# Optimization experiments

Measured on AMD Instinct MI355X. Metric: run time of the kernel, lower is better.

Reference implementation:

```python
import jax, jax.numpy as jnp
import numpy as np

HIDDEN = 2048
VOCAB = 32768
SEQ = 4608
N_CHUNKS = 9
CAP = 30.0
IGNORE = -100


def setup_inputs() -> dict:
    key = jax.random.key(0)
    k1, k2, k3 = jax.random.split(key, 3)
    weight = (jax.random.normal(k1, (VOCAB, HIDDEN), dtype=jnp.float32) * 0.02).astype(jnp.bfloat16)
    hidden = jax.random.normal(k2, (1, SEQ, HIDDEN), dtype=jnp.float32)
    input_ids = jax.random.randint(k3, (1, SEQ), 0, VOCAB)
    attention_mask = jnp.ones((1, SEQ), dtype=jnp.int32)
    return {"weight": weight, "hidden": hidden, "input_ids": input_ids,
            "attention_mask": attention_mask}


def _build_labels(input_ids, attention_mask):
    # labels[t] = input_ids[t+1], masked-out positions and the final position -> -100
    ids = input_ids[0]
    am = attention_mask[0]
    lab = jnp.where(am[1:] == 0, IGNORE, ids[1:])            # [S-1]
    lab = jnp.concatenate([lab, jnp.full((1,), IGNORE, lab.dtype)])  # [S]
    return lab


def reference(weight, hidden, input_ids, attention_mask):
    labels = _build_labels(input_ids, attention_mask)        # [S]
    x = hidden.reshape(-1, HIDDEN)                           # [S, H] fp32
    chunk = SEQ // N_CHUNKS
    xs = x.reshape(N_CHUNKS, chunk, HIDDEN)
    ls = labels.reshape(N_CHUNKS, chunk)

    wT = weight.T                                            # [H, V] bf16

    def chunk_loss(args):
        xc, lc = args                                        # [c,H], [c]
        # softcapped logits: CAP * tanh((x @ W^T) / CAP), mm in bf16
        t = jnp.tanh((xc.astype(jnp.bfloat16) @ wT) / CAP).astype(jnp.float32)  # [c,V]
        z = CAP * (t - jnp.max(t, axis=1, keepdims=True))    # stable shifted logits
        logp = z - jnp.log(jnp.sum(jnp.exp(z), axis=1, keepdims=True))
        valid = lc != IGNORE
        idx = jnp.where(valid, lc, 0)
        nll = -jnp.take_along_axis(logp, idx[:, None], axis=1)[:, 0]
        return jnp.sum(jnp.where(valid, nll, 0.0))

    losses = jax.lax.map(chunk_loss, (xs, ls))               # [N_CHUNKS]
    return jnp.sum(losses)
```

## Files before the change

### kernel.cpp

```cpp
#include <hip/hip_runtime.h>
#include <hip/hip_bf16.h>
#include <cstdint>

#define S_LEN   4608
#define HID     2048
#define VOCAB_N 32768
#define CAPV    30.0f
#define IGNORE_IDX (-100)
#define NT512   512

typedef short bf16x8 __attribute__((ext_vector_type(8)));
typedef float f32x4  __attribute__((ext_vector_type(4)));

__device__ __forceinline__ unsigned short f2bf_rtne(float f) {
    unsigned int u = __float_as_uint(f);
    unsigned int r = u + 0x7fffu + ((u >> 16) & 1u);
    return (unsigned short)(r >> 16);
}
__device__ __forceinline__ float bf_lo(unsigned int u) { return __uint_as_float(u << 16); }
__device__ __forceinline__ float bf_hi(unsigned int u) { return __uint_as_float(u & 0xffff0000u); }
__device__ __forceinline__ float bfdot2(unsigned int x, unsigned int w) {
    return bf_lo(x) * bf_lo(w) + bf_hi(x) * bf_hi(w);
}
__device__ __forceinline__ float softcap(float logit) {
    float e = __expf(logit * (2.0f / CAPV));
    return CAPV * (e - 1.0f) / (e + 1.0f);
}

__global__ void cvt_kernel(const float* __restrict__ h, unsigned short* __restrict__ xb) {
    int i = blockIdx.x * blockDim.x + threadIdx.x;
    float4 v = ((const float4*)h)[i];
    ushort4 o;
    o.x = f2bf_rtne(v.x); o.y = f2bf_rtne(v.y);
    o.z = f2bf_rtne(v.z); o.w = f2bf_rtne(v.w);
    ((ushort4*)xb)[i] = o;
}

__global__ __launch_bounds__(256)
void gemm_lse_kernel(const unsigned short* __restrict__ X,
                     const unsigned short* __restrict__ W,
                     float* __restrict__ partL) {
    __shared__ __align__(16) unsigned short As[128 * 32];
    __shared__ __align__(16) unsigned short Bs[128 * 32];

    const int tid  = threadIdx.x;
    const int wave = tid >> 6;
    const int lane = tid & 63;
    const int tileM = blockIdx.y * 128;
    const int tileN = blockIdx.x * 128;

    const int lr = lane >> 2;
    const int lc = (lane & 3) * 8;

    const unsigned short* Abase = X + (size_t)(tileM + wave * 32) * HID;
    const unsigned short* Bbase = W + (size_t)(tileN + wave * 32) * HID;

    const int wr  = wave >> 1, wc = wave & 1;
    const int q   = lane >> 4, l16 = lane & 15;

    f32x4 acc[4][4] = {};

    for (int k0 = 0; k0 < HID; k0 += 32) {
        __syncthreads();
        #pragma unroll
        for (int j = 0; j < 2; ++j) {
            const unsigned short* ga = Abase + (size_t)(j * 16 + lr) * HID + k0 + lc;
            __builtin_amdgcn_global_load_lds(
                (const __attribute__((address_space(1))) void*)ga,
                (__attribute__((address_space(3))) void*)&As[(wave * 32 + j * 16) * 32],
                16, 0, 0);
            const unsigned short* gb = Bbase + (size_t)(j * 16 + lr) * HID + k0 + lc;
            __builtin_amdgcn_global_load_lds(
                (const __attribute__((address_space(1))) void*)gb,
                (__attribute__((address_space(3))) void*)&Bs[(wave * 32 + j * 16) * 32],
                16, 0, 0);
        }
        __syncthreads();

        bf16x8 av[4], bv[4];
        #pragma unroll
        for (int t = 0; t < 4; ++t) {
            av[t] = *(const bf16x8*)&As[(wr * 64 + t * 16 + l16) * 32 + q * 8];
            bv[t] = *(const bf16x8*)&Bs[(wc * 64 + t * 16 + l16) * 32 + q * 8];
        }
        #pragma unroll
        for (int ti = 0; ti < 4; ++ti)
            #pragma unroll
            for (int tj = 0; tj < 4; ++tj)
                acc[ti][tj] = __builtin_amdgcn_mfma_f32_16x16x32_bf16(
                    av[ti], bv[tj], acc[ti][tj], 0, 0, 0);
    }

    const int rowbase = tileM + wr * 64;
    const int ntile   = blockIdx.x * 2 + wc;
    #pragma unroll
    for (int ti = 0; ti < 4; ++ti) {
        #pragma unroll
        for (int r = 0; r < 4; ++r) {
            float s = 0.0f;
            #pragma unroll
            for (int tj = 0; tj < 4; ++tj)
                s += __expf(softcap(acc[ti][tj][r]));
            s += __shfl_xor(s, 1);
            s += __shfl_xor(s, 2);
            s += __shfl_xor(s, 4);
            s += __shfl_xor(s, 8);
            if (l16 == 0)
                partL[(size_t)(rowbase + ti * 16 + q * 4 + r) * NT512 + ntile] = s;
        }
    }
}

__global__ void row_reduce_kernel(const unsigned short* __restrict__ X,
                                  const unsigned short* __restrict__ W,
                                  const int* __restrict__ ids,
                                  const int* __restrict__ am,
                                  const float* __restrict__ partL,
                                  float* __restrict__ row_loss) {
    const int wave = threadIdx.x >> 6;
    const int lane = threadIdx.x & 63;
    const int r = blockIdx.x * 4 + wave;

    int lab = IGNORE_IDX;
    if (r < S_LEN - 1 && am[r + 1] != 0) lab = ids[r + 1];
    const bool valid = (lab >= 0 && lab < VOCAB_N);

    float dot = 0.0f;
    if (valid) {
        const unsigned short* xr = X + (size_t)r   * HID;
        const unsigned short* wr = W + (size_t)lab * HID;
        #pragma unroll
        for (int c = 0; c < 4; ++c) {
            const int off = c * 512 + lane * 8;
            uint4 xu = *(const uint4*)(xr + off);
            uint4 wu = *(const uint4*)(wr + off);
            dot += bfdot2(xu.x, wu.x) + bfdot2(xu.y, wu.y) +
                   bfdot2(xu.z, wu.z) + bfdot2(xu.w, wu.w);
        }
    }
    #pragma unroll
    for (int m = 1; m < 64; m <<= 1) dot += __shfl_xor(dot, m);

    float L = 0.0f;
    const float* pr = partL + (size_t)r * NT512;
    #pragma unroll
    for (int i = 0; i < 8; ++i) L += pr[i * 64 + lane];
    #pragma unroll
    for (int m = 1; m < 64; m <<= 1) L += __shfl_xor(L, m);

    if (lane == 0) {
        float loss = 0.0f;
        if (valid) loss = logf(L) - softcap(dot);
        row_loss[r] = loss;
    }
}

__global__ void final_sum_kernel(const float* __restrict__ row_loss, float* __restrict__ out) {
    __shared__ float sm[256];
    float s = 0.0f;
    for (int i = threadIdx.x; i < S_LEN; i += 256) s += row_loss[i];
    sm[threadIdx.x] = s;
    __syncthreads();
    for (int st = 128; st > 0; st >>= 1) {
        if (threadIdx.x < st) sm[threadIdx.x] += sm[threadIdx.x + st];
        __syncthreads();
    }
    if (threadIdx.x == 0) out[0] = sm[0];
}

extern "C" void kernel_launch(void* const* d_in, const int* in_sizes, int n_in,
                              void* d_out, int out_size, void* d_ws, size_t ws_size,
                              hipStream_t stream) {
    const unsigned short* W  = (const unsigned short*)d_in[0];
    const float*  hidden     = (const float*)d_in[1];
    const int*    ids        = (const int*)d_in[2];
    const int*    am         = (const int*)d_in[3];
    float* out = (float*)d_out;

    char* ws = (char*)d_ws;
    unsigned short* Xb   = (unsigned short*)ws;
    float* partL         = (float*)(ws + (size_t)S_LEN * HID * 2);
    float* row_loss      = (float*)(ws + (size_t)S_LEN * HID * 2
                                       + (size_t)S_LEN * NT512 * 4);

    cvt_kernel<<<(S_LEN * HID / 4) / 256, 256, 0, stream>>>(hidden, Xb);

    dim3 g(VOCAB_N / 128, S_LEN / 128);
    gemm_lse_kernel<<<g, 256, 0, stream>>>(Xb, W, partL);

    row_reduce_kernel<<<S_LEN / 4, 256, 0, stream>>>(Xb, W, ids, am, partL, row_loss);

    final_sum_kernel<<<1, 256, 0, stream>>>(row_loss, out);
}
```

Measured before the change: 1.074 ms.

## Widen GEMM K-tile to 64 with XOR-swizzled LDS, fuse final reduction via atomics

```diff
diff --git a/kernel.cpp b/kernel.cpp
--- a/kernel.cpp
+++ b/kernel.cpp
@@ -17,14 +17,22 @@
     unsigned int r = u + 0x7fffu + ((u >> 16) & 1u);
     return (unsigned short)(r >> 16);
 }
+__device__ __forceinline__ float bfr(float f) {
+    unsigned int u = __float_as_uint(f);
+    unsigned int r = u + 0x7fffu + ((u >> 16) & 1u);
+    return __uint_as_float(r & 0xffff0000u);
+}
 __device__ __forceinline__ float bf_lo(unsigned int u) { return __uint_as_float(u << 16); }
 __device__ __forceinline__ float bf_hi(unsigned int u) { return __uint_as_float(u & 0xffff0000u); }
 __device__ __forceinline__ float bfdot2(unsigned int x, unsigned int w) {
     return bf_lo(x) * bf_lo(w) + bf_hi(x) * bf_hi(w);
 }
-__device__ __forceinline__ float softcap(float logit) {
-    float e = __expf(logit * (2.0f / CAPV));
-    return CAPV * (e - 1.0f) / (e + 1.0f);
+__device__ __forceinline__ float softcap_ref(float logit) {
+    float lb = bfr(logit);
+    float x  = bfr(lb / CAPV);
+    float e  = __expf(2.0f * x);
+    float t  = bfr((e - 1.0f) / (e + 1.0f));
+    return CAPV * t;
 }
 
 __global__ void cvt_kernel(const float* __restrict__ h, unsigned short* __restrict__ xb) {
@@ -40,8 +48,8 @@
 void gemm_lse_kernel(const unsigned short* __restrict__ X,
                      const unsigned short* __restrict__ W,
                      float* __restrict__ partL) {
-    __shared__ __align__(16) unsigned short As[128 * 32];
-    __shared__ __align__(16) unsigned short Bs[128 * 32];
+    __shared__ __align__(16) unsigned short As[128 * 64];
+    __shared__ __align__(16) unsigned short Bs[128 * 64];
 
     const int tid  = threadIdx.x;
     const int wave = tid >> 6;
@@ -49,46 +57,60 @@
     const int tileM = blockIdx.y * 128;
     const int tileN = blockIdx.x * 128;
 
-    const int lr = lane >> 2;
-    const int lc = (lane & 3) * 8;
-
-    const unsigned short* Abase = X + (size_t)(tileM + wave * 32) * HID;
-    const unsigned short* Bbase = W + (size_t)(tileN + wave * 32) * HID;
+    const int r8 = lane >> 3;
+    const int s8 = lane & 7;
+    const int cg = s8 ^ r8;
+
+    const unsigned short* Abase = X + (size_t)(tileM + wave * 32) * HID + cg * 8;
+    const unsigned short* Bbase = W + (size_t)(tileN + wave * 32) * HID + cg * 8;
 
     const int wr  = wave >> 1, wc = wave & 1;
     const int q   = lane >> 4, l16 = lane & 15;
 
+    const int c0 = ((q)     ^ (l16 & 7)) * 8;
+    const int c1 = ((4 | q) ^ (l16 & 7)) * 8;
+    int arow[4], brow[4];
+    #pragma unroll
+    for (int t = 0; t < 4; ++t) {
+        arow[t] = (wr * 64 + t * 16 + l16) * 64;
+        brow[t] = (wc * 64 + t * 16 + l16) * 64;
+    }
+
     f32x4 acc[4][4] = {};
 
-    for (int k0 = 0; k0 < HID; k0 += 32) {
+    for (int k0 = 0; k0 < HID; k0 += 64) {
         __syncthreads();
         #pragma unroll
-        for (int j = 0; j < 2; ++j) {
-            const unsigned short* ga = Abase + (size_t)(j * 16 + lr) * HID + k0 + lc;
+        for (int j = 0; j < 4; ++j) {
+            const unsigned short* ga = Abase + (size_t)(j * 8 + r8) * HID + k0;
             __builtin_amdgcn_global_load_lds(
                 (const __attribute__((address_space(1))) void*)ga,
-                (__attribute__((address_space(3))) void*)&As[(wave * 32 + j * 16) * 32],
+                (__attribute__((address_space(3))) void*)&As[(wave * 32 + j * 8) * 64],
                 16, 0, 0);
-            const unsigned short* gb = Bbase + (size_t)(j * 16 + lr) * HID + k0 + lc;
+            const unsigned short* gb = Bbase + (size_t)(j * 8 + r8) * HID + k0;
             __builtin_amdgcn_global_load_lds(
                 (const __attribute__((address_space(1))) void*)gb,
-                (__attribute__((address_space(3))) void*)&Bs[(wave * 32 + j * 16) * 32],
+                (__attribute__((address_space(3))) void*)&Bs[(wave * 32 + j * 8) * 64],
                 16, 0, 0);
         }
         __syncthreads();
 
-        bf16x8 av[4], bv[4];
-        #pragma unroll
-        for (int t = 0; t < 4; ++t) {
-            av[t] = *(const bf16x8*)&As[(wr * 64 + t * 16 + l16) * 32 + q * 8];
-            bv[t] = *(const bf16x8*)&Bs[(wc * 64 + t * 16 + l16) * 32 + q * 8];
-        }
-        #pragma unroll
-        for (int ti = 0; ti < 4; ++ti)
+        #pragma unroll
+        for (int kk = 0; kk < 2; ++kk) {
+            const int cs = kk ? c1 : c0;
+            bf16x8 av[4], bv[4];
             #pragma unroll
-            for (int tj = 0; tj < 4; ++tj)
-                acc[ti][tj] = __builtin_amdgcn_mfma_f32_16x16x32_bf16(
-                    av[ti], bv[tj], acc[ti][tj], 0, 0, 0);
+            for (int t = 0; t < 4; ++t) {
+                av[t] = *(const bf16x8*)&As[arow[t] + cs];
+                bv[t] = *(const bf16x8*)&Bs[brow[t] + cs];
+            }
+            #pragma unroll
+            for (int ti = 0; ti < 4; ++ti)
+                #pragma unroll
+                for (int tj = 0; tj < 4; ++tj)
+                    acc[ti][tj] = __builtin_amdgcn_mfma_f32_16x16x32_bf16(
+                        av[ti], bv[tj], acc[ti][tj], 0, 0, 0);
+        }
     }
 
     const int rowbase = tileM + wr * 64;
@@ -100,7 +122,7 @@
             float s = 0.0f;
             #pragma unroll
             for (int tj = 0; tj < 4; ++tj)
-                s += __expf(softcap(acc[ti][tj][r]));
+                s += __expf(softcap_ref(acc[ti][tj][r]));
             s += __shfl_xor(s, 1);
             s += __shfl_xor(s, 2);
             s += __shfl_xor(s, 4);
@@ -116,7 +138,8 @@
                                   const int* __restrict__ ids,
                                   const int* __restrict__ am,
                                   const float* __restrict__ partL,
-                                  float* __restrict__ row_loss) {
+                                  float* __restrict__ out) {
+    __shared__ float blk[4];
     const int wave = threadIdx.x >> 6;
     const int lane = threadIdx.x & 63;
     const int r = blockIdx.x * 4 + wave;
@@ -150,22 +173,12 @@
 
     if (lane == 0) {
         float loss = 0.0f;
-        if (valid) loss = logf(L) - softcap(dot);
-        row_loss[r] = loss;
-    }
-}
-
-__global__ void final_sum_kernel(const float* __restrict__ row_loss, float* __restrict__ out) {
-    __shared__ float sm[256];
-    float s = 0.0f;
-    for (int i = threadIdx.x; i < S_LEN; i += 256) s += row_loss[i];
-    sm[threadIdx.x] = s;
+        if (valid) loss = logf(L) - softcap_ref(dot);
+        blk[wave] = loss;
+    }
     __syncthreads();
-    for (int st = 128; st > 0; st >>= 1) {
-        if (threadIdx.x < st) sm[threadIdx.x] += sm[threadIdx.x + st];
-        __syncthreads();
-    }
-    if (threadIdx.x == 0) out[0] = sm[0];
+    if (threadIdx.x == 0)
+        atomicAdd(out, blk[0] + blk[1] + blk[2] + blk[3]);
 }
 
 extern "C" void kernel_launch(void* const* d_in, const int* in_sizes, int n_in,
@@ -178,17 +191,15 @@
     float* out = (float*)d_out;
 
     char* ws = (char*)d_ws;
-    unsigned short* Xb   = (unsigned short*)ws;
-    float* partL         = (float*)(ws + (size_t)S_LEN * HID * 2);
-    float* row_loss      = (float*)(ws + (size_t)S_LEN * HID * 2
-                                       + (size_t)S_LEN * NT512 * 4);
+    unsigned short* Xb = (unsigned short*)ws;
+    float* partL       = (float*)(ws + (size_t)S_LEN * HID * 2);
+
+    hipMemsetAsync(out, 0, (size_t)out_size * 4, stream);
 
     cvt_kernel<<<(S_LEN * HID / 4) / 256, 256, 0, stream>>>(hidden, Xb);
 
     dim3 g(VOCAB_N / 128, S_LEN / 128);
     gemm_lse_kernel<<<g, 256, 0, stream>>>(Xb, W, partL);
 
-    row_reduce_kernel<<<S_LEN / 4, 256, 0, stream>>>(Xb, W, ids, am, partL, row_loss);
-
-    final_sum_kernel<<<1, 256, 0, stream>>>(row_loss, out);
-}
+    row_reduce_kernel<<<S_LEN / 4, 256, 0, stream>>>(Xb, W, ids, am, partL, out);
+}
```

New measurement: 1.208 ms. 12.5% more time.
